# Kernel optimization log

Hardware: AMD Instinct MI355X
Metric: run time of the kernel (lower is better)

## Reference

```python
import jax, jax.numpy as jnp
import numpy as np

B, K, L, H = 64, 32, 64, 256


def setup_inputs() -> dict:
    key = jax.random.key(0)
    ks = jax.random.split(key, 24)
    def rnd(i, shape, scale):
        return jax.random.normal(ks[i], shape, dtype=jnp.float32) * scale
    s = 0.05  # small init for weights to keep activations sane
    return {
        'h_ue': rnd(0, (B, K, H), 1.0),
        'h_ap': rnd(1, (B, L, H), 1.0),
        'e':    rnd(2, (B, L * K, H), 1.0),
        # msg_ap_to_ue: Linear(2H->H), Linear(H->H)
        'a2u_w1': rnd(3, (H, 2 * H), s), 'a2u_b1': rnd(4, (H,), s),
        'a2u_w2': rnd(5, (H, H), s),     'a2u_b2': rnd(6, (H,), s),
        # msg_ue_to_ap
        'u2a_w1': rnd(7, (H, 2 * H), s), 'u2a_b1': rnd(8, (H,), s),
        'u2a_w2': rnd(9, (H, H), s),     'u2a_b2': rnd(10, (H,), s),
        # GRUCell (PyTorch layout: weight_ih (3H,H), weight_hh (3H,H))
        'ue_wih': rnd(11, (3 * H, H), s), 'ue_bih': rnd(12, (3 * H,), s),
        'ue_whh': rnd(13, (3 * H, H), s), 'ue_bhh': rnd(14, (3 * H,), s),
        'ap_wih': rnd(15, (3 * H, H), s), 'ap_bih': rnd(16, (3 * H,), s),
        'ap_whh': rnd(17, (3 * H, H), s), 'ap_bhh': rnd(18, (3 * H,), s),
        # edge_update: Linear(3H->H), Linear(H->H)
        'ed_w1': rnd(19, (H, 3 * H), s), 'ed_b1': rnd(20, (H,), s),
        'ed_w2': rnd(21, (H, H), s),     'ed_b2': rnd(22, (H,), s),
    }


def _gru(x, h, wih, bih, whh, bhh):
    # PyTorch GRUCell semantics
    gi = jnp.einsum('...h,oh->...o', x, wih) + bih
    gh = jnp.einsum('...h,oh->...o', h, whh) + bhh
    i_r, i_z, i_n = jnp.split(gi, 3, axis=-1)
    h_r, h_z, h_n = jnp.split(gh, 3, axis=-1)
    r = jax.nn.sigmoid(i_r + h_r)
    z = jax.nn.sigmoid(i_z + h_z)
    n = jnp.tanh(i_n + r * h_n)
    return (1.0 - z) * n + z * h


def reference(h_ue, h_ap, e,
              a2u_w1, a2u_b1, a2u_w2, a2u_b2,
              u2a_w1, u2a_b1, u2a_w2, u2a_b2,
              ue_wih, ue_bih, ue_whh, ue_bhh,
              ap_wih, ap_bih, ap_whh, ap_bhh,
              ed_w1, ed_b1, ed_w2, ed_b2):
    Bd, Kd, Hd = h_ue.shape
    Ld = h_ap.shape[1]
    e4 = e.reshape(Bd, Ld, Kd, Hd)  # edge (b, l, k) on dense bipartite graph

    # --- AP -> UE messages: MLP(concat[h_ap_src, e]); split first linear ---
    pre = (jnp.einsum('blh,oh->blo', h_ap, a2u_w1[:, :Hd])[:, :, None, :]
           + jnp.einsum('blkh,oh->blko', e4, a2u_w1[:, Hd:]) + a2u_b1)
    msg = jnp.einsum('blkh,oh->blko', jax.nn.relu(pre), a2u_w2) + a2u_b2
    m_ue = msg.mean(axis=1)  # mean over AP neighbors -> (B,K,H)

    # --- UE -> AP messages ---
    pre = (jnp.einsum('bkh,oh->bko', h_ue, u2a_w1[:, :Hd])[:, None, :, :]
           + jnp.einsum('blkh,oh->blko', e4, u2a_w1[:, Hd:]) + u2a_b1)
    msg = jnp.einsum('blkh,oh->blko', jax.nn.relu(pre), u2a_w2) + u2a_b2
    m_ap = msg.mean(axis=2)  # mean over UE neighbors -> (B,L,H)

    # --- GRU node updates ---
    h_ue_new = _gru(m_ue, h_ue, ue_wih, ue_bih, ue_whh, ue_bhh)
    h_ap_new = _gru(m_ap, h_ap, ap_wih, ap_bih, ap_whh, ap_bhh)

    # --- edge update: MLP(concat[src=UE_new, dst=AP_new, e]) ---
    pre = (jnp.einsum('bkh,oh->bko', h_ue_new, ed_w1[:, :Hd])[:, None, :, :]
           + jnp.einsum('blh,oh->blo', h_ap_new, ed_w1[:, Hd:2 * Hd])[:, :, None, :]
           + jnp.einsum('blkh,oh->blko', e4, ed_w1[:, 2 * Hd:]) + ed_b1)
    e_new = jnp.einsum('blkh,oh->blko', jax.nn.relu(pre), ed_w2) + ed_b2

    return h_ue_new, h_ap_new, e_new.reshape(Bd, Ld * Kd, Hd)
```

## Files before the change

### kernel.cpp

```cpp
#include <hip/hip_runtime.h>

#define HH 256
#define BB 64
#define KK 32
#define LL 64
#define LGRP 8

typedef __bf16 bf16_t;
typedef __attribute__((ext_vector_type(8))) __bf16 bf16x8;
typedef __attribute__((ext_vector_type(4))) float f32x4;

__device__ __forceinline__ bf16x8 ld_a8(const float* __restrict__ p) {
  const f32x4* q = (const f32x4*)p;
  f32x4 a = q[0], b = q[1];
  bf16x8 r;
  r[0] = (__bf16)a[0]; r[1] = (__bf16)a[1]; r[2] = (__bf16)a[2]; r[3] = (__bf16)a[3];
  r[4] = (__bf16)b[0]; r[5] = (__bf16)b[1]; r[6] = (__bf16)b[2]; r[7] = (__bf16)b[3];
  return r;
}

__device__ __forceinline__ void ld_tile(const float* __restrict__ E, int tid, f32x4 r[4]) {
  const f32x4* q = (const f32x4*)(E + tid * 16);
  r[0] = q[0]; r[1] = q[1]; r[2] = q[2]; r[3] = q[3];
}
__device__ __forceinline__ void wr_tile(bf16_t* buf, int tid, const f32x4 r[4]) {
  int row = tid >> 4;
  int colb = (tid & 15) * 32;
  bf16x8 v0, v1;
  v0[0] = (__bf16)r[0][0]; v0[1] = (__bf16)r[0][1]; v0[2] = (__bf16)r[0][2]; v0[3] = (__bf16)r[0][3];
  v0[4] = (__bf16)r[1][0]; v0[5] = (__bf16)r[1][1]; v0[6] = (__bf16)r[1][2]; v0[7] = (__bf16)r[1][3];
  v1[0] = (__bf16)r[2][0]; v1[1] = (__bf16)r[2][1]; v1[2] = (__bf16)r[2][2]; v1[3] = (__bf16)r[2][3];
  v1[4] = (__bf16)r[3][0]; v1[5] = (__bf16)r[3][1]; v1[6] = (__bf16)r[3][2]; v1[7] = (__bf16)r[3][3];
  int swz = (row & 7) << 4;
  *(bf16x8*)((char*)buf + row * 512 + (colb ^ swz)) = v0;
  *(bf16x8*)((char*)buf + row * 512 + ((colb + 16) ^ swz)) = v1;
}

template<int LDB, int NT>
__device__ __forceinline__ void mm_f32A(const float* __restrict__ A,
                                        const bf16_t* __restrict__ B,
                                        f32x4 acc[2][NT], int lane) {
  const int c = lane & 15, g = lane >> 4;
#pragma unroll
  for (int ks = 0; ks < 8; ++ks) {
    const int ko = ks * 32 + g * 8;
    bf16x8 a0 = ld_a8(A + (size_t)c * HH + ko);
    bf16x8 a1 = ld_a8(A + (size_t)(16 + c) * HH + ko);
#pragma unroll
    for (int nt = 0; nt < NT; ++nt) {
      bf16x8 bb = *(const bf16x8*)(B + (size_t)(nt * 16 + c) * LDB + ko);
      acc[0][nt] = __builtin_amdgcn_mfma_f32_16x16x32_bf16(a0, bb, acc[0][nt], 0, 0, 0);
      acc[1][nt] = __builtin_amdgcn_mfma_f32_16x16x32_bf16(a1, bb, acc[1][nt], 0, 0, 0);
    }
  }
}

__global__ __launch_bounds__(256) void prep_kernel(
    const float* w0, const float* w1, const float* w2, const float* w3,
    const float* w4, const float* w5, const float* w6, const float* w7,
    const float* w8, const float* w9, bf16_t* wb) {
  int i = blockIdx.x * 256 + threadIdx.x;
  const float* s; int o; float sc = 1.f;
  if      (i < 131072)  { s = w0; o = i; }
  else if (i < 196608)  { s = w1; o = i - 131072; sc = 1.f / 64.f; }
  else if (i < 327680)  { s = w2; o = i - 196608; }
  else if (i < 393216)  { s = w3; o = i - 327680; sc = 1.f / 32.f; }
  else if (i < 589824)  { s = w4; o = i - 393216; }
  else if (i < 786432)  { s = w5; o = i - 589824; }
  else if (i < 983040)  { s = w6; o = i - 786432; }
  else if (i < 1179648) { s = w7; o = i - 983040; }
  else if (i < 1376256) { s = w8; o = i - 1179648; }
  else                  { s = w9; o = i - 1376256; }
  wb[i] = (__bf16)(s[o] * sc);
}

template<int LDW>
__global__ __launch_bounds__(256) void proj2h_kernel(
    const float* __restrict__ X0, const bf16_t* __restrict__ W0,
    const float* __restrict__ b0, float* __restrict__ out0, int n0,
    const float* __restrict__ X1, const bf16_t* __restrict__ W1,
    const float* __restrict__ b1, float* __restrict__ out1) {
  const int t = blockIdx.x >> 1, ch = blockIdx.x & 1;
  const float* X; const bf16_t* W; const float* bias; float* out; int row0;
  if (t < n0) { X = X0; W = W0; bias = b0; out = out0; row0 = t * 32; }
  else        { X = X1; W = W1; bias = b1; out = out1; row0 = (t - n0) * 32; }
  const int tid = threadIdx.x, w = tid >> 6, lane = tid & 63;
  const int colw = ch * 128 + w * 32, c = lane & 15, g = lane >> 4;
  f32x4 acc[2][2];
#pragma unroll
  for (int nt = 0; nt < 2; ++nt) {
    float bv = bias ? bias[colw + nt * 16 + c] : 0.f;
    f32x4 v = {bv, bv, bv, bv};
    acc[0][nt] = v; acc[1][nt] = v;
  }
  mm_f32A<LDW, 2>(X + (size_t)row0 * HH, W + (size_t)colw * LDW, acc, lane);
#pragma unroll
  for (int m = 0; m < 2; ++m)
#pragma unroll
    for (int nt = 0; nt < 2; ++nt)
#pragma unroll
      for (int rr = 0; rr < 4; ++rr) {
        int row = row0 + m * 16 + g * 4 + rr;
        out[(size_t)row * HH + colw + nt * 16 + c] = acc[m][nt][rr];
      }
}

__global__ __launch_bounds__(512) void phaseA_kernel(
    const float* __restrict__ e, const float* __restrict__ p_ap,
    const float* __restrict__ p_ue,
    const bf16_t* __restrict__ wu1e, const bf16_t* __restrict__ wa1e,
    float* __restrict__ part, float* __restrict__ R_ap) {
  __shared__ bf16_t ebuf[2][32 * 256];
  const int blk = blockIdx.x;
  const int b = blk >> 3, lc = blk & 7;
  const int tid = threadIdx.x, w = tid >> 6, lane = tid & 63;
  const int colw = w * 32, c = lane & 15, g = lane >> 4;
  const int l0 = lc * LGRP;

  bf16x8 wU[2][8], wA[2][8];
#pragma unroll
  for (int nt = 0; nt < 2; ++nt)
#pragma unroll
    for (int ks = 0; ks < 8; ++ks) {
      size_t off = (size_t)(colw + nt * 16 + c) * 512 + ks * 32 + g * 8;
      wU[nt][ks] = *(const bf16x8*)(wu1e + off);
      wA[nt][ks] = *(const bf16x8*)(wa1e + off);
    }

  float pue[2][2][4];
#pragma unroll
  for (int m = 0; m < 2; ++m)
#pragma unroll
    for (int nt = 0; nt < 2; ++nt)
#pragma unroll
      for (int rr = 0; rr < 4; ++rr)
        pue[m][nt][rr] = p_ue[(size_t)(b * KK + m * 16 + g * 4 + rr) * HH + colw + nt * 16 + c];

  f32x4 accU[2][2];
  const f32x4 z4 = {0.f, 0.f, 0.f, 0.f};
#pragma unroll
  for (int m = 0; m < 2; ++m)
#pragma unroll
    for (int nt = 0; nt < 2; ++nt) accU[m][nt] = z4;

  f32x4 rs[4];
  ld_tile(e + (size_t)((b * LL + l0) * KK) * HH, tid, rs);
  wr_tile(ebuf[0], tid, rs);

  for (int li = 0; li < LGRP; ++li) {
    __syncthreads();
    const int l = l0 + li;
    if (li + 1 < LGRP) ld_tile(e + (size_t)((b * LL + l + 1) * KK) * HH, tid, rs);

    f32x4 aU[2][2], aA[2][2];
#pragma unroll
    for (int nt = 0; nt < 2; ++nt) {
      float pa = p_ap[(size_t)(b * LL + l) * HH + colw + nt * 16 + c];
      f32x4 t = {pa, pa, pa, pa};
      aA[0][nt] = t; aA[1][nt] = t;
#pragma unroll
      for (int rr = 0; rr < 4; ++rr) {
        aU[0][nt][rr] = pue[0][nt][rr];
        aU[1][nt][rr] = pue[1][nt][rr];
      }
    }
    const bf16_t* eb = ebuf[li & 1];
    const int swz = (c & 7) << 4;
#pragma unroll
    for (int ks = 0; ks < 8; ++ks) {
      const int kb = (ks * 32 + g * 8) * 2;
      bf16x8 a0 = *(const bf16x8*)((const char*)eb + c * 512 + (kb ^ swz));
      bf16x8 a1 = *(const bf16x8*)((const char*)eb + (16 + c) * 512 + (kb ^ swz));
#pragma unroll
      for (int nt = 0; nt < 2; ++nt) {
        aU[0][nt] = __builtin_amdgcn_mfma_f32_16x16x32_bf16(a0, wU[nt][ks], aU[0][nt], 0, 0, 0);
        aU[1][nt] = __builtin_amdgcn_mfma_f32_16x16x32_bf16(a1, wU[nt][ks], aU[1][nt], 0, 0, 0);
        aA[0][nt] = __builtin_amdgcn_mfma_f32_16x16x32_bf16(a0, wA[nt][ks], aA[0][nt], 0, 0, 0);
        aA[1][nt] = __builtin_amdgcn_mfma_f32_16x16x32_bf16(a1, wA[nt][ks], aA[1][nt], 0, 0, 0);
      }
    }

#pragma unroll
    for (int nt = 0; nt < 2; ++nt) {
      float s = 0.f;
#pragma unroll
      for (int m = 0; m < 2; ++m)
#pragma unroll
        for (int rr = 0; rr < 4; ++rr) s += fmaxf(aU[m][nt][rr], 0.f);
      s += __shfl_xor(s, 16);
      s += __shfl_xor(s, 32);
      if (lane < 16)
        R_ap[(size_t)(b * LL + l) * HH + colw + nt * 16 + lane] = s;
    }
#pragma unroll
    for (int m = 0; m < 2; ++m)
#pragma unroll
      for (int nt = 0; nt < 2; ++nt)
#pragma unroll
        for (int rr = 0; rr < 4; ++rr)
          accU[m][nt][rr] += fmaxf(aA[m][nt][rr], 0.f);

    if (li + 1 < LGRP) wr_tile(ebuf[(li + 1) & 1], tid, rs);
  }

#pragma unroll
  for (int m = 0; m < 2; ++m)
#pragma unroll
    for (int nt = 0; nt < 2; ++nt)
#pragma unroll
      for (int rr = 0; rr < 4; ++rr) {
        int krow = m * 16 + g * 4 + rr;
        part[(size_t)((lc * BB + b) * KK + krow) * HH + colw + nt * 16 + c] = accU[m][nt][rr];
      }
}

__global__ __launch_bounds__(256) void reduce_kernel(
    const float* __restrict__ part, float* __restrict__ R_ue) {
  int i = blockIdx.x * 256 + threadIdx.x;
  float s = 0.f;
#pragma unroll
  for (int lc = 0; lc < 8; ++lc) s += part[(size_t)lc * 524288 + i];
  R_ue[i] = s;
}

__global__ __launch_bounds__(256) void gru_kernel(
    const float* __restrict__ m_ue, const float* __restrict__ h_ue,
    const bf16_t* __restrict__ wih_ue, const bf16_t* __restrict__ whh_ue,
    const float* __restrict__ ue_bih, const float* __restrict__ ue_bhh,
    float* __restrict__ hue_new,
    const float* __restrict__ m_ap, const float* __restrict__ h_ap,
    const bf16_t* __restrict__ wih_ap, const bf16_t* __restrict__ whh_ap,
    const float* __restrict__ ap_bih, const float* __restrict__ ap_bhh,
    float* __restrict__ hap_new) {
  const int t = blockIdx.x >> 1, ch = blockIdx.x & 1;
  const float *x, *h, *bih, *bhh; const bf16_t *wih, *whh; float* hout; int row0;
  if (t < 64) { x = m_ue; h = h_ue; wih = wih_ue; whh = whh_ue;
                bih = ue_bih; bhh = ue_bhh; hout = hue_new; row0 = t * 32; }
  else        { x = m_ap; h = h_ap; wih = wih_ap; whh = whh_ap;
                bih = ap_bih; bhh = ap_bhh; hout = hap_new; row0 = (t - 64) * 32; }
  const int tid = threadIdx.x, w = tid >> 6, lane = tid & 63;
  const int colw = ch * 128 + w * 32, c = lane & 15, g = lane >> 4;
  f32x4 aR[2][2], aZ[2][2], aN[2][2], aHN[2][2];
#pragma unroll
  for (int nt = 0; nt < 2; ++nt) {
    int col = colw + nt * 16 + c;
    float vR = bih[col] + bhh[col];
    float vZ = bih[256 + col] + bhh[256 + col];
    float vN = bih[512 + col];
    float vH = bhh[512 + col];
    f32x4 tR = {vR, vR, vR, vR}, tZ = {vZ, vZ, vZ, vZ};
    f32x4 tN = {vN, vN, vN, vN}, tH = {vH, vH, vH, vH};
    aR[0][nt] = tR; aR[1][nt] = tR;
    aZ[0][nt] = tZ; aZ[1][nt] = tZ;
    aN[0][nt] = tN; aN[1][nt] = tN;
    aHN[0][nt] = tH; aHN[1][nt] = tH;
  }
  const float* X = x + (size_t)row0 * HH;
  const float* Hp = h + (size_t)row0 * HH;
  mm_f32A<256, 2>(X,  wih + (size_t)(0   + colw) * 256, aR, lane);
  mm_f32A<256, 2>(Hp, whh + (size_t)(0   + colw) * 256, aR, lane);
  mm_f32A<256, 2>(X,  wih + (size_t)(256 + colw) * 256, aZ, lane);
  mm_f32A<256, 2>(Hp, whh + (size_t)(256 + colw) * 256, aZ, lane);
  mm_f32A<256, 2>(X,  wih + (size_t)(512 + colw) * 256, aN, lane);
  mm_f32A<256, 2>(Hp, whh + (size_t)(512 + colw) * 256, aHN, lane);
#pragma unroll
  for (int m = 0; m < 2; ++m)
#pragma unroll
    for (int nt = 0; nt < 2; ++nt)
#pragma unroll
      for (int rr = 0; rr < 4; ++rr) {
        int row = row0 + m * 16 + g * 4 + rr;
        int col = colw + nt * 16 + c;
        float rg = 1.f / (1.f + __expf(-aR[m][nt][rr]));
        float zg = 1.f / (1.f + __expf(-aZ[m][nt][rr]));
        float tv = aN[m][nt][rr] + rg * aHN[m][nt][rr];
        tv = fminf(fmaxf(tv, -15.f), 15.f);
        float ex = __expf(-2.f * tv);
        float ng = (1.f - ex) / (1.f + ex);
        float ho = h[(size_t)row * HH + col];
        hout[(size_t)row * HH + col] = (1.f - zg) * ng + zg * ho;
      }
}

__global__ __launch_bounds__(512) void phaseC_kernel(
    const float* __restrict__ e, const float* __restrict__ q_ue,
    const float* __restrict__ q_ap,
    const bf16_t* __restrict__ wed1e, const bf16_t* __restrict__ wed2,
    const float* __restrict__ ed_b2, float* __restrict__ e_new) {
  __shared__ bf16_t ebuf[2][32 * 256];
  __shared__ bf16_t pbuf[2][32 * 256];
  const int blk = blockIdx.x;
  const int b = blk >> 3, lc = blk & 7;
  const int tid = threadIdx.x, w = tid >> 6, lane = tid & 63;
  const int colw = w * 32, c = lane & 15, g = lane >> 4;
  const int l0 = lc * LGRP;

  bf16x8 w1[2][8], w2[2][8];
#pragma unroll
  for (int nt = 0; nt < 2; ++nt)
#pragma unroll
    for (int ks = 0; ks < 8; ++ks) {
      w1[nt][ks] = *(const bf16x8*)(wed1e + (size_t)(colw + nt * 16 + c) * 768 + ks * 32 + g * 8);
      w2[nt][ks] = *(const bf16x8*)(wed2  + (size_t)(colw + nt * 16 + c) * 256 + ks * 32 + g * 8);
    }

  float qU[2][2][4];
#pragma unroll
  for (int m = 0; m < 2; ++m)
#pragma unroll
    for (int nt = 0; nt < 2; ++nt)
#pragma unroll
      for (int rr = 0; rr < 4; ++rr)
        qU[m][nt][rr] = q_ue[(size_t)(b * KK + m * 16 + g * 4 + rr) * HH + colw + nt * 16 + c];
  float b2v[2];
#pragma unroll
  for (int nt = 0; nt < 2; ++nt) b2v[nt] = ed_b2[colw + nt * 16 + c];

  const int swz = (c & 7) << 4;

  f32x4 rs[4];
  ld_tile(e + (size_t)((b * LL + l0) * KK) * HH, tid, rs);
  wr_tile(ebuf[0], tid, rs);

  for (int li = 0; li < LGRP; ++li) {
    __syncthreads();
    const int l = l0 + li;
    if (li + 1 < LGRP) ld_tile(e + (size_t)((b * LL + l + 1) * KK) * HH, tid, rs);

    if (li > 0) {
      const bf16_t* pb = pbuf[(li - 1) & 1];
      f32x4 a2[2][2];
#pragma unroll
      for (int nt = 0; nt < 2; ++nt) {
        f32x4 t = {b2v[nt], b2v[nt], b2v[nt], b2v[nt]};
        a2[0][nt] = t; a2[1][nt] = t;
      }
#pragma unroll
      for (int ks = 0; ks < 8; ++ks) {
        const int kb = (ks * 32 + g * 8) * 2;
        bf16x8 a0 = *(const bf16x8*)((const char*)pb + c * 512 + (kb ^ swz));
        bf16x8 a1f = *(const bf16x8*)((const char*)pb + (16 + c) * 512 + (kb ^ swz));
#pragma unroll
        for (int nt = 0; nt < 2; ++nt) {
          a2[0][nt] = __builtin_amdgcn_mfma_f32_16x16x32_bf16(a0,  w2[nt][ks], a2[0][nt], 0, 0, 0);
          a2[1][nt] = __builtin_amdgcn_mfma_f32_16x16x32_bf16(a1f, w2[nt][ks], a2[1][nt], 0, 0, 0);
        }
      }
#pragma unroll
      for (int m = 0; m < 2; ++m)
#pragma unroll
        for (int nt = 0; nt < 2; ++nt)
#pragma unroll
          for (int rr = 0; rr < 4; ++rr) {
            int row = m * 16 + g * 4 + rr;
            int col = colw + nt * 16 + c;
            e_new[(size_t)((b * LL + l - 1) * KK + row) * HH + col] = a2[m][nt][rr];
          }
    }

    f32x4 a1[2][2];
#pragma unroll
    for (int nt = 0; nt < 2; ++nt) {
      float qa = q_ap[(size_t)(b * LL + l) * HH + colw + nt * 16 + c];
#pragma unroll
      for (int rr = 0; rr < 4; ++rr) {
        a1[0][nt][rr] = qa + qU[0][nt][rr];
        a1[1][nt][rr] = qa + qU[1][nt][rr];
      }
    }
    const bf16_t* eb = ebuf[li & 1];
#pragma unroll
    for (int ks = 0; ks < 8; ++ks) {
      const int kb = (ks * 32 + g * 8) * 2;
      bf16x8 a0 = *(const bf16x8*)((const char*)eb + c * 512 + (kb ^ swz));
      bf16x8 a1f = *(const bf16x8*)((const char*)eb + (16 + c) * 512 + (kb ^ swz));
#pragma unroll
      for (int nt = 0; nt < 2; ++nt) {
        a1[0][nt] = __builtin_amdgcn_mfma_f32_16x16x32_bf16(a0,  w1[nt][ks], a1[0][nt], 0, 0, 0);
        a1[1][nt] = __builtin_amdgcn_mfma_f32_16x16x32_bf16(a1f, w1[nt][ks], a1[1][nt], 0, 0, 0);
      }
    }
    bf16_t* pw = pbuf[li & 1];
#pragma unroll
    for (int m = 0; m < 2; ++m)
#pragma unroll
      for (int nt = 0; nt < 2; ++nt)
#pragma unroll
        for (int rr = 0; rr < 4; ++rr) {
          int row = m * 16 + g * 4 + rr;
          int col = colw + nt * 16 + c;
          float v = fmaxf(a1[m][nt][rr], 0.f);
          int off = row * 512 + ((col * 2) ^ ((row & 7) << 4));
          *(bf16_t*)((char*)pw + off) = (__bf16)v;
        }

    if (li + 1 < LGRP) wr_tile(ebuf[(li + 1) & 1], tid, rs);
  }

  __syncthreads();
  {
    const bf16_t* pb = pbuf[(LGRP - 1) & 1];
    f32x4 a2[2][2];
#pragma unroll
    for (int nt = 0; nt < 2; ++nt) {
      f32x4 t = {b2v[nt], b2v[nt], b2v[nt], b2v[nt]};
      a2[0][nt] = t; a2[1][nt] = t;
    }
#pragma unroll
    for (int ks = 0; ks < 8; ++ks) {
      const int kb = (ks * 32 + g * 8) * 2;
      bf16x8 a0 = *(const bf16x8*)((const char*)pb + c * 512 + (kb ^ swz));
      bf16x8 a1f = *(const bf16x8*)((const char*)pb + (16 + c) * 512 + (kb ^ swz));
#pragma unroll
      for (int nt = 0; nt < 2; ++nt) {
        a2[0][nt] = __builtin_amdgcn_mfma_f32_16x16x32_bf16(a0,  w2[nt][ks], a2[0][nt], 0, 0, 0);
        a2[1][nt] = __builtin_amdgcn_mfma_f32_16x16x32_bf16(a1f, w2[nt][ks], a2[1][nt], 0, 0, 0);
      }
    }
#pragma unroll
    for (int m = 0; m < 2; ++m)
#pragma unroll
      for (int nt = 0; nt < 2; ++nt)
#pragma unroll
        for (int rr = 0; rr < 4; ++rr) {
          int row = m * 16 + g * 4 + rr;
          int col = colw + nt * 16 + c;
          e_new[(size_t)((b * LL + l0 + LGRP - 1) * KK + row) * HH + col] = a2[m][nt][rr];
        }
  }
}

extern "C" void kernel_launch(void* const* d_in, const int* in_sizes, int n_in,
                              void* d_out, int out_size, void* d_ws, size_t ws_size,
                              hipStream_t stream) {
  const float* h_ue   = (const float*)d_in[0];
  const float* h_ap   = (const float*)d_in[1];
  const float* e      = (const float*)d_in[2];
  const float* a2u_w1 = (const float*)d_in[3];
  const float* a2u_b1 = (const float*)d_in[4];
  const float* a2u_w2 = (const float*)d_in[5];
  const float* a2u_b2 = (const float*)d_in[6];
  const float* u2a_w1 = (const float*)d_in[7];
  const float* u2a_b1 = (const float*)d_in[8];
  const float* u2a_w2 = (const float*)d_in[9];
  const float* u2a_b2 = (const float*)d_in[10];
  const float* ue_wih = (const float*)d_in[11];
  const float* ue_bih = (const float*)d_in[12];
  const float* ue_whh = (const float*)d_in[13];
  const float* ue_bhh = (const float*)d_in[14];
  const float* ap_wih = (const float*)d_in[15];
  const float* ap_bih = (const float*)d_in[16];
  const float* ap_whh = (const float*)d_in[17];
  const float* ap_bhh = (const float*)d_in[18];
  const float* ed_w1  = (const float*)d_in[19];
  const float* ed_b1  = (const float*)d_in[20];
  const float* ed_w2  = (const float*)d_in[21];
  const float* ed_b2  = (const float*)d_in[22];

  bf16_t* wb      = (bf16_t*)d_ws;
  bf16_t* wa1     = wb;
  bf16_t* wa2s    = wa1 + 131072;
  bf16_t* wu1     = wa2s + 65536;
  bf16_t* wu2s    = wu1 + 131072;
  bf16_t* wih_ue  = wu2s + 65536;
  bf16_t* whh_ue  = wih_ue + 196608;
  bf16_t* wih_ap  = whh_ue + 196608;
  bf16_t* whh_ap  = wih_ap + 196608;
  bf16_t* wed1    = whh_ap + 196608;
  bf16_t* wed2    = wed1 + 196608;
  float* fbase = (float*)((char*)d_ws + 2883584);
  float* m_ue = fbase;
  float* m_ap = m_ue + 524288;
  float* p_ap = m_ap + 1048576;
  float* p_ue = p_ap + 1048576;
  float* q_ue = p_ue + 524288;
  float* q_ap = q_ue + 524288;
  float* part = q_ap + 1048576;
  float* R_ue = q_ue;
  float* R_ap = q_ap;

  float* out      = (float*)d_out;
  float* hue_new  = out;
  float* hap_new  = out + 524288;
  float* e_new    = out + 1572864;

  prep_kernel<<<5632, 256, 0, stream>>>(a2u_w1, a2u_w2, u2a_w1, u2a_w2,
                                        ue_wih, ue_whh, ap_wih, ap_whh,
                                        ed_w1, ed_w2, wb);
  proj2h_kernel<512><<<384, 256, 0, stream>>>(h_ap, wa1, a2u_b1, p_ap, 128,
                                              h_ue, wu1, u2a_b1, p_ue);
  phaseA_kernel<<<512, 512, 0, stream>>>(e, p_ap, p_ue, wu1 + 256, wa1 + 256,
                                         part, R_ap);
  reduce_kernel<<<2048, 256, 0, stream>>>(part, R_ue);
  proj2h_kernel<256><<<384, 256, 0, stream>>>(R_ue, wa2s, a2u_b2, m_ue, 64,
                                              R_ap, wu2s, u2a_b2, m_ap);
  gru_kernel<<<384, 256, 0, stream>>>(m_ue, h_ue, wih_ue, whh_ue, ue_bih, ue_bhh, hue_new,
                                      m_ap, h_ap, wih_ap, whh_ap, ap_bih, ap_bhh, hap_new);
  proj2h_kernel<768><<<384, 256, 0, stream>>>(hue_new, wed1, ed_b1, q_ue, 64,
                                              hap_new, wed1 + 256, nullptr, q_ap);
  phaseC_kernel<<<512, 512, 0, stream>>>(e, q_ue, q_ap, wed1 + 512, wed2, ed_b2, e_new);
}
```

Measured before the change: 216.1 us.

## Fuse message projection, GRU update and edge node projection into one kernel

Replaces three launches (second-layer message projection, GRU cell, and node projections for the edge MLP) with a single node2_kernel. Each block handles 32 rows across all 256 columns and keeps intermediate m and h_new in swizzled LDS as bf16, so they no longer round-trip through global memory. This removes two kernel launches and the associated global traffic. The cost is a grid that shrinks from 384 to 192 blocks with more serial work per block, which may underuse the GPU's compute units.

```diff
diff --git a/kernel.cpp b/kernel.cpp
--- a/kernel.cpp
+++ b/kernel.cpp
@@ -49,6 +49,26 @@
 #pragma unroll
     for (int nt = 0; nt < NT; ++nt) {
       bf16x8 bb = *(const bf16x8*)(B + (size_t)(nt * 16 + c) * LDB + ko);
+      acc[0][nt] = __builtin_amdgcn_mfma_f32_16x16x32_bf16(a0, bb, acc[0][nt], 0, 0, 0);
+      acc[1][nt] = __builtin_amdgcn_mfma_f32_16x16x32_bf16(a1, bb, acc[1][nt], 0, 0, 0);
+    }
+  }
+}
+
+template<int LDB, int NT>
+__device__ __forceinline__ void mm_ldsA(const bf16_t* lds,
+                                        const bf16_t* __restrict__ B,
+                                        f32x4 acc[2][NT], int lane) {
+  const int c = lane & 15, g = lane >> 4;
+  const int swz = (c & 7) << 4;
+#pragma unroll
+  for (int ks = 0; ks < 8; ++ks) {
+    const int kb = (ks * 32 + g * 8) * 2;
+    bf16x8 a0 = *(const bf16x8*)((const char*)lds + c * 512 + (kb ^ swz));
+    bf16x8 a1 = *(const bf16x8*)((const char*)lds + (16 + c) * 512 + (kb ^ swz));
+#pragma unroll
+    for (int nt = 0; nt < NT; ++nt) {
+      bf16x8 bb = *(const bf16x8*)(B + (size_t)(nt * 16 + c) * LDB + ks * 32 + g * 8);
       acc[0][nt] = __builtin_amdgcn_mfma_f32_16x16x32_bf16(a0, bb, acc[0][nt], 0, 0, 0);
       acc[1][nt] = __builtin_amdgcn_mfma_f32_16x16x32_bf16(a1, bb, acc[1][nt], 0, 0, 0);
     }
@@ -223,26 +243,62 @@
   R_ue[i] = s;
 }
 
-__global__ __launch_bounds__(256) void gru_kernel(
-    const float* __restrict__ m_ue, const float* __restrict__ h_ue,
-    const bf16_t* __restrict__ wih_ue, const bf16_t* __restrict__ whh_ue,
-    const float* __restrict__ ue_bih, const float* __restrict__ ue_bhh,
-    float* __restrict__ hue_new,
-    const float* __restrict__ m_ap, const float* __restrict__ h_ap,
-    const bf16_t* __restrict__ wih_ap, const bf16_t* __restrict__ whh_ap,
-    const float* __restrict__ ap_bih, const float* __restrict__ ap_bhh,
-    float* __restrict__ hap_new) {
-  const int t = blockIdx.x >> 1, ch = blockIdx.x & 1;
-  const float *x, *h, *bih, *bhh; const bf16_t *wih, *whh; float* hout; int row0;
-  if (t < 64) { x = m_ue; h = h_ue; wih = wih_ue; whh = whh_ue;
-                bih = ue_bih; bhh = ue_bhh; hout = hue_new; row0 = t * 32; }
-  else        { x = m_ap; h = h_ap; wih = wih_ap; whh = whh_ap;
-                bih = ap_bih; bhh = ap_bhh; hout = hap_new; row0 = (t - 64) * 32; }
+__global__ __launch_bounds__(256) void node2_kernel(
+    const float* __restrict__ R_ue, const float* __restrict__ R_ap,
+    const bf16_t* __restrict__ wa2s, const float* __restrict__ a2u_b2,
+    const bf16_t* __restrict__ wu2s, const float* __restrict__ u2a_b2,
+    const float* __restrict__ h_ue, const bf16_t* __restrict__ wih_ue,
+    const float* __restrict__ ue_bih, const bf16_t* __restrict__ whh_ue,
+    const float* __restrict__ ue_bhh,
+    const float* __restrict__ h_ap, const bf16_t* __restrict__ wih_ap,
+    const float* __restrict__ ap_bih, const bf16_t* __restrict__ whh_ap,
+    const float* __restrict__ ap_bhh,
+    const bf16_t* __restrict__ wed1, const float* __restrict__ ed_b1,
+    float* __restrict__ hue_new, float* __restrict__ hap_new,
+    float* __restrict__ q_ue, float* __restrict__ q_ap) {
+  __shared__ bf16_t mbuf[32 * 256];
+  __shared__ bf16_t hbuf[32 * 256];
+  const int blk = blockIdx.x;
+  const bool ue = blk < 64;
+  const int row0 = ue ? blk * 32 : (blk - 64) * 32;
   const int tid = threadIdx.x, w = tid >> 6, lane = tid & 63;
-  const int colw = ch * 128 + w * 32, c = lane & 15, g = lane >> 4;
-  f32x4 aR[2][2], aZ[2][2], aN[2][2], aHN[2][2];
-#pragma unroll
-  for (int nt = 0; nt < 2; ++nt) {
+  const int colw = w * 64, c = lane & 15, g = lane >> 4;
+  const float*  R   = ue ? R_ue : R_ap;
+  const bf16_t* W2  = ue ? wa2s : wu2s;
+  const float*  b2  = ue ? a2u_b2 : u2a_b2;
+  const float*  h   = ue ? h_ue : h_ap;
+  const bf16_t* wih = ue ? wih_ue : wih_ap;
+  const bf16_t* whh = ue ? whh_ue : whh_ap;
+  const float*  bih = ue ? ue_bih : ap_bih;
+  const float*  bhh = ue ? ue_bhh : ap_bhh;
+  float* hout = ue ? hue_new : hap_new;
+  float* qout = ue ? q_ue : q_ap;
+  const bf16_t* wq = wed1 + (ue ? 0 : 256);
+
+  f32x4 acc[2][4];
+#pragma unroll
+  for (int nt = 0; nt < 4; ++nt) {
+    float bv = b2[colw + nt * 16 + c];
+    f32x4 t = {bv, bv, bv, bv};
+    acc[0][nt] = t; acc[1][nt] = t;
+  }
+  mm_f32A<256, 4>(R + (size_t)row0 * HH, W2 + (size_t)colw * 256, acc, lane);
+#pragma unroll
+  for (int m = 0; m < 2; ++m)
+#pragma unroll
+    for (int nt = 0; nt < 4; ++nt)
+#pragma unroll
+      for (int rr = 0; rr < 4; ++rr) {
+        int row = m * 16 + g * 4 + rr;
+        int col = colw + nt * 16 + c;
+        int off = row * 512 + ((col * 2) ^ ((row & 7) << 4));
+        *(bf16_t*)((char*)mbuf + off) = (__bf16)acc[m][nt][rr];
+      }
+  __syncthreads();
+
+  f32x4 aR[2][4], aZ[2][4], aN[2][4], aHN[2][4];
+#pragma unroll
+  for (int nt = 0; nt < 4; ++nt) {
     int col = colw + nt * 16 + c;
     float vR = bih[col] + bhh[col];
     float vZ = bih[256 + col] + bhh[256 + col];
@@ -255,21 +311,20 @@
     aN[0][nt] = tN; aN[1][nt] = tN;
     aHN[0][nt] = tH; aHN[1][nt] = tH;
   }
-  const float* X = x + (size_t)row0 * HH;
   const float* Hp = h + (size_t)row0 * HH;
-  mm_f32A<256, 2>(X,  wih + (size_t)(0   + colw) * 256, aR, lane);
-  mm_f32A<256, 2>(Hp, whh + (size_t)(0   + colw) * 256, aR, lane);
-  mm_f32A<256, 2>(X,  wih + (size_t)(256 + colw) * 256, aZ, lane);
-  mm_f32A<256, 2>(Hp, whh + (size_t)(256 + colw) * 256, aZ, lane);
-  mm_f32A<256, 2>(X,  wih + (size_t)(512 + colw) * 256, aN, lane);
-  mm_f32A<256, 2>(Hp, whh + (size_t)(512 + colw) * 256, aHN, lane);
-#pragma unroll
-  for (int m = 0; m < 2; ++m)
-#pragma unroll
-    for (int nt = 0; nt < 2; ++nt)
-#pragma unroll
-      for (int rr = 0; rr < 4; ++rr) {
-        int row = row0 + m * 16 + g * 4 + rr;
+  mm_ldsA<256, 4>(mbuf, wih + (size_t)(0   + colw) * 256, aR, lane);
+  mm_f32A<256, 4>(Hp,  whh + (size_t)(0   + colw) * 256, aR, lane);
+  mm_ldsA<256, 4>(mbuf, wih + (size_t)(256 + colw) * 256, aZ, lane);
+  mm_f32A<256, 4>(Hp,  whh + (size_t)(256 + colw) * 256, aZ, lane);
+  mm_ldsA<256, 4>(mbuf, wih + (size_t)(512 + colw) * 256, aN, lane);
+  mm_f32A<256, 4>(Hp,  whh + (size_t)(512 + colw) * 256, aHN, lane);
+#pragma unroll
+  for (int m = 0; m < 2; ++m)
+#pragma unroll
+    for (int nt = 0; nt < 4; ++nt)
+#pragma unroll
+      for (int rr = 0; rr < 4; ++rr) {
+        int row = m * 16 + g * 4 + rr;
         int col = colw + nt * 16 + c;
         float rg = 1.f / (1.f + __expf(-aR[m][nt][rr]));
         float zg = 1.f / (1.f + __expf(-aZ[m][nt][rr]));
@@ -277,8 +332,30 @@
         tv = fminf(fmaxf(tv, -15.f), 15.f);
         float ex = __expf(-2.f * tv);
         float ng = (1.f - ex) / (1.f + ex);
-        float ho = h[(size_t)row * HH + col];
-        hout[(size_t)row * HH + col] = (1.f - zg) * ng + zg * ho;
+        float ho = h[(size_t)(row0 + row) * HH + col];
+        float hn = (1.f - zg) * ng + zg * ho;
+        hout[(size_t)(row0 + row) * HH + col] = hn;
+        int off = row * 512 + ((col * 2) ^ ((row & 7) << 4));
+        *(bf16_t*)((char*)hbuf + off) = (__bf16)hn;
+      }
+  __syncthreads();
+
+  f32x4 aq[2][4];
+#pragma unroll
+  for (int nt = 0; nt < 4; ++nt) {
+    float bv = ue ? ed_b1[colw + nt * 16 + c] : 0.f;
+    f32x4 t = {bv, bv, bv, bv};
+    aq[0][nt] = t; aq[1][nt] = t;
+  }
+  mm_ldsA<768, 4>(hbuf, wq + (size_t)colw * 768, aq, lane);
+#pragma unroll
+  for (int m = 0; m < 2; ++m)
+#pragma unroll
+    for (int nt = 0; nt < 4; ++nt)
+#pragma unroll
+      for (int rr = 0; rr < 4; ++rr) {
+        int row = row0 + m * 16 + g * 4 + rr;
+        qout[(size_t)row * HH + colw + nt * 16 + c] = aq[m][nt][rr];
       }
 }
 
@@ -476,7 +553,7 @@
   float* q_ue = p_ue + 524288;
   float* q_ap = q_ue + 524288;
   float* part = q_ap + 1048576;
-  float* R_ue = q_ue;
+  float* R_ue = m_ue;
   float* R_ap = q_ap;
 
   float* out      = (float*)d_out;
@@ -492,11 +569,11 @@
   phaseA_kernel<<<512, 512, 0, stream>>>(e, p_ap, p_ue, wu1 + 256, wa1 + 256,
                                          part, R_ap);
   reduce_kernel<<<2048, 256, 0, stream>>>(part, R_ue);
-  proj2h_kernel<256><<<384, 256, 0, stream>>>(R_ue, wa2s, a2u_b2, m_ue, 64,
-                                              R_ap, wu2s, u2a_b2, m_ap);
-  gru_kernel<<<384, 256, 0, stream>>>(m_ue, h_ue, wih_ue, whh_ue, ue_bih, ue_bhh, hue_new,
-                                      m_ap, h_ap, wih_ap, whh_ap, ap_bih, ap_bhh, hap_new);
-  proj2h_kernel<768><<<384, 256, 0, stream>>>(hue_new, wed1, ed_b1, q_ue, 64,
-                                              hap_new, wed1 + 256, nullptr, q_ap);
+  node2_kernel<<<192, 256, 0, stream>>>(R_ue, R_ap,
+                                        wa2s, a2u_b2, wu2s, u2a_b2,
+                                        h_ue, wih_ue, ue_bih, whh_ue, ue_bhh,
+                                        h_ap, wih_ap, ap_bih, whh_ap, ap_bhh,
+                                        wed1, ed_b1,
+                                        hue_new, hap_new, q_ue, q_ap);
   phaseC_kernel<<<512, 512, 0, stream>>>(e, q_ue, q_ap, wed1 + 512, wed2, ed_b2, e_new);
 }
```

Result: faster. 198.3 us, median of 2 (-8.2%).
